# Optimization experiments

Hardware: AMD Instinct MI355X
Metric: run time of the kernel (lower is better)

Reference implementation:

```python
import jax, jax.numpy as jnp
import numpy as np

N_WAY = 64

def setup_inputs() -> dict:
    key = jax.random.key(0)
    k1, k2, k3, k4 = jax.random.split(key, 4)
    S, Q, F, D = 1024, 16384, 2048, 512
    xs = jax.random.normal(k1, (S, F), dtype=jnp.float32)
    ys = jax.random.randint(k2, (S,), 0, N_WAY, dtype=jnp.int64)
    xq = jax.random.normal(k3, (Q, F), dtype=jnp.float32)
    W = jax.random.normal(k4, (F, D), dtype=jnp.float32) * 0.02
    b = jnp.zeros((D,), dtype=jnp.float32)
    return {"xs": xs, "ys": ys, "xq": xq, "W": W, "b": b}

def reference(xs, ys, xq, W, b):
    # encoder: linear projection [*, F] -> [*, D]
    z_s = xs @ W + b            # [S, D]
    z_q = xq @ W + b            # [Q, D]
    # class prototypes: segment mean over support embeddings -> [N_way, D]
    counts = jax.ops.segment_sum(jnp.ones_like(ys, dtype=z_s.dtype), ys, num_segments=N_WAY)
    proto = jax.ops.segment_sum(z_s, ys, num_segments=N_WAY) / jnp.clip(counts, 1.0)[:, None]
    # pairwise squared euclidean distance (expand + pow + sum), [Q, N_way]
    diff = z_q[:, None, :] - proto[None, :, :]   # [Q, N_way, D]
    dists = jnp.sum(diff * diff, axis=-1)
    return -dists
```

## Files before the change

kernel.cpp:

```cpp
#include <hip/hip_runtime.h>


typedef __attribute__((ext_vector_type(8))) short short8;
typedef __attribute__((ext_vector_type(4))) float floatx4;

#define S_ROWS 1024
#define F_DIM  2048
#define D_DIM  512
#define NWAY   64
#define Q_ROWS 16384

static __device__ __forceinline__ unsigned short f2bf(float f) {
  unsigned int u = __float_as_uint(f);
  u += 0x7FFF + ((u >> 16) & 1);
  return (unsigned short)(u >> 16);
}
static __device__ __forceinline__ float bf2f(unsigned short s) {
  return __uint_as_float(((unsigned int)s) << 16);
}
static __device__ __forceinline__ unsigned int pack_bf2(float x, float y) {
  unsigned int ux = __float_as_uint(x) + 0x8000u;
  unsigned int uy = __float_as_uint(y) + 0x8000u;
  return __builtin_amdgcn_perm(uy, ux, 0x07060302u);
}
static __device__ __forceinline__ void load_lds16(const unsigned short* g, unsigned short* l) {
  __builtin_amdgcn_global_load_lds((const __attribute__((address_space(1))) unsigned int*)g,
                                   (__attribute__((address_space(3))) unsigned int*)l,
                                   16, 0, 0);
}

__global__ __launch_bounds__(256) void k_prep(const float* __restrict__ W,
                                              unsigned short* __restrict__ Wt,
                                              const int* __restrict__ ys,
                                              int* __restrict__ order,
                                              int* __restrict__ starts,
                                              float* __restrict__ counts) {
  __shared__ unsigned short t[64][65];
  __shared__ int cnt[NWAY];
  __shared__ int st[NWAY + 1];
  __shared__ int wp[NWAY];
  int bx = blockIdx.x;
  int tid = threadIdx.x;
  if (bx < 256) {
    int f0 = (bx >> 3) << 6;
    int d0 = (bx & 7) << 6;
    for (int j = 0; j < 16; j++) {
      int lin = j * 256 + tid;
      int fl = lin >> 6, dl = lin & 63;
      t[fl][dl] = f2bf(W[(size_t)(f0 + fl) * D_DIM + d0 + dl]);
    }
    __syncthreads();
    for (int j = 0; j < 16; j++) {
      int lin = j * 256 + tid;
      int dl = lin >> 6, fl = lin & 63;
      Wt[(size_t)(d0 + dl) * F_DIM + f0 + fl] = t[fl][dl];
    }
  } else {
    if (tid < NWAY) cnt[tid] = 0;
    __syncthreads();
    for (int j = tid; j < S_ROWS; j += 256) atomicAdd(&cnt[ys[j]], 1);
    __syncthreads();
    if (tid == 0) {
      int a = 0;
      for (int c = 0; c < NWAY; c++) { st[c] = a; wp[c] = a; a += cnt[c]; }
      st[NWAY] = a;
    }
    __syncthreads();
    for (int j = tid; j < S_ROWS; j += 256) {
      int c = ys[j];
      int p = atomicAdd(&wp[c], 1);
      order[p] = j;
    }
    if (tid < NWAY) counts[tid] = (float)cnt[tid];
    if (tid < NWAY + 1) starts[tid] = st[tid];
  }
}

__global__ __launch_bounds__(256) void k1_csum(const float* __restrict__ xs,
                                               const int* __restrict__ order,
                                               const int* __restrict__ starts,
                                               float* __restrict__ csum) {
  __shared__ int lord[S_ROWS];
  int c = blockIdx.x >> 1;
  int tid = threadIdx.x;
  int s = starts[c], e = starts[c + 1];
  int len = e - s;
  for (int j = tid; j < len; j += 256) lord[j] = order[s + j];
  __syncthreads();
  int f0 = (blockIdx.x & 1) * 1024 + tid * 4;
  float4 a = {0.f, 0.f, 0.f, 0.f};
  for (int i = 0; i < len; i++) {
    float4 v = *(const float4*)&xs[(size_t)lord[i] * F_DIM + f0];
    a.x += v.x; a.y += v.y; a.z += v.z; a.w += v.w;
  }
  *(float4*)&csum[(size_t)c * F_DIM + f0] = a;
}

__global__ __launch_bounds__(256) void k2p(const float* __restrict__ W,
                                           const float* __restrict__ csum,
                                           float* __restrict__ proto_part) {
  __shared__ __align__(16) float csl[64 * 65];
  __shared__ __align__(16) float wch[64 * 64];
  int bx = blockIdx.x;
  int fg = bx >> 3, dc = bx & 7;
  int d0 = dc * 64;
  int tid = threadIdx.x;
  int c = tid >> 2, dq = (tid & 3) * 16;
  floatx4 a0 = {0.f,0.f,0.f,0.f}, a1 = a0, a2 = a0, a3 = a0;
  for (int fsub = 0; fsub < 4; fsub++) {
    int f0 = (fg * 4 + fsub) * 64;
    __syncthreads();
    for (int idx = tid; idx < 4096; idx += 256) {
      int r = idx >> 6, q = idx & 63;
      csl[r * 65 + q] = csum[(size_t)r * F_DIM + f0 + q];
      wch[idx] = W[(size_t)(f0 + r) * D_DIM + d0 + q];
    }
    __syncthreads();
#pragma unroll 4
    for (int f = 0; f < 64; f++) {
      float s = csl[c * 65 + f];
      const floatx4* wr = (const floatx4*)&wch[f * 64 + dq];
      floatx4 w0 = wr[0], w1 = wr[1], w2 = wr[2], w3 = wr[3];
      a0 += s * w0; a1 += s * w1; a2 += s * w2; a3 += s * w3;
    }
  }
  float* dst = &proto_part[((size_t)fg * NWAY + c) * D_DIM + d0 + dq];
  *(floatx4*)&dst[0]  = a0;
  *(floatx4*)&dst[4]  = a1;
  *(floatx4*)&dst[8]  = a2;
  *(floatx4*)&dst[12] = a3;
}

__global__ __launch_bounds__(256) void k_pfin(const float* __restrict__ proto_part,
                                              const float* __restrict__ b,
                                              const float* __restrict__ counts,
                                              unsigned short* __restrict__ proto_bf,
                                              float* __restrict__ pnorm) {
  __shared__ float red[256];
  int n = blockIdx.x, tid = threadIdx.x;
  float cntv = counts[n];
  float inv = 1.f / fmaxf(cntv, 1.f);
  float part = 0.f;
#pragma unroll
  for (int h = 0; h < 2; h++) {
    int d = h * 256 + tid;
    float raw = 0.f;
#pragma unroll
    for (int p = 0; p < 8; p++)
      raw += proto_part[((size_t)p * NWAY + n) * D_DIM + d];
    float pv = (raw + cntv * b[d]) * inv;
    unsigned short hh = f2bf(pv);
    proto_bf[(size_t)n * D_DIM + d] = hh;
    float q = bf2f(hh);
    part += q * q;
  }
  red[tid] = part;
  __syncthreads();
  for (int s = 128; s > 0; s >>= 1) {
    if (tid < s) red[tid] += red[tid + s];
    __syncthreads();
  }
  if (tid == 0) pnorm[n] = red[0];
}

__global__ __launch_bounds__(256) void k3_gemm(const float* __restrict__ xq,
                                               const unsigned short* __restrict__ Wt,
                                               const float* __restrict__ b,
                                               unsigned short* __restrict__ zbuf) {
  __shared__ __align__(16) unsigned short lA[128 * 64];
  __shared__ __align__(16) unsigned short lB[128 * 64];
  int tid = threadIdx.x;
  int bx = blockIdx.x;
  int xcd = bx & 7;
  int wg = xcd * 64 + (bx >> 3);
  int mt = wg >> 2;
  int n0 = (wg & 3) * 128;

  int wave = tid >> 6, lane = tid & 63;
  int wr = wave >> 1, wc = wave & 1;
  int lrow = lane & 15, lquad = lane >> 4;

  const float* Ab = xq + (size_t)mt * 128 * F_DIM;

  floatx4 acc[4][4];
#pragma unroll
  for (int i = 0; i < 4; i++)
#pragma unroll
    for (int j = 0; j < 4; j++) acc[i][j] = (floatx4){0.f, 0.f, 0.f, 0.f};

  int sr = tid >> 3, skq = tid & 7;
  const float* ag = Ab + (size_t)sr * F_DIM + skq * 8;
  const unsigned short* bg = Wt + (size_t)(n0 + sr) * F_DIM + skq * 8;

  for (int k0 = 0; k0 < F_DIM; k0 += 64) {
#pragma unroll
    for (int i = 0; i < 4; i++)
      load_lds16(bg + (size_t)i * 32 * F_DIM + k0, &lB[(i * 256 + wave * 64) * 8]);
#pragma unroll
    for (int p = 0; p < 4; p++) {
      const float* gp = ag + (size_t)p * 32 * F_DIM + k0;
      float4 v0 = *(const float4*)gp;
      float4 v1 = *(const float4*)(gp + 4);
      uint4 w;
      w.x = pack_bf2(v0.x, v0.y); w.y = pack_bf2(v0.z, v0.w);
      w.z = pack_bf2(v1.x, v1.y); w.w = pack_bf2(v1.z, v1.w);
      *(uint4*)&lA[(p * 256 + tid) * 8] = w;
    }
    __syncthreads();
#pragma unroll
    for (int s = 0; s < 2; s++) {
      short8 af[4], bfr[4];
#pragma unroll
      for (int i = 0; i < 4; i++)
        af[i] = *(const short8*)&lA[(wr * 64 + i * 16 + lrow) * 64 + s * 32 + lquad * 8];
#pragma unroll
      for (int j = 0; j < 4; j++)
        bfr[j] = *(const short8*)&lB[(wc * 64 + j * 16 + lrow) * 64 + s * 32 + lquad * 8];
#pragma unroll
      for (int i = 0; i < 4; i++)
#pragma unroll
        for (int j = 0; j < 4; j++)
          acc[i][j] = __builtin_amdgcn_mfma_f32_16x16x32_bf16(af[i], bfr[j], acc[i][j], 0, 0, 0);
    }
    __syncthreads();
  }

  size_t zr0 = (size_t)mt * 128;
#pragma unroll
  for (int j = 0; j < 4; j++) {
    int col = n0 + wc * 64 + j * 16 + lrow;
    float bb = b[col];
#pragma unroll
    for (int i = 0; i < 4; i++) {
#pragma unroll
      for (int r = 0; r < 4; r++) {
        int row = wr * 64 + i * 16 + lquad * 4 + r;
        zbuf[(zr0 + row) * D_DIM + col] = f2bf(acc[i][j][r] + bb);
      }
    }
  }
}

__global__ __launch_bounds__(256) void k5_dist(const unsigned short* __restrict__ zbuf,
                                               const unsigned short* __restrict__ proto_bf,
                                               const float* __restrict__ pnorm,
                                               float* __restrict__ out) {
  __shared__ float S[64 * 65];
  __shared__ float qn_l[64];
  __shared__ float pn_l[64];
  int tid = threadIdx.x;
  int q0 = blockIdx.x * 64;
  int wave = tid >> 6, lane = tid & 63;
  int lrow = lane & 15, lquad = lane >> 4;

  for (int i = tid; i < 64 * 65; i += 256) S[i] = 0.f;
  if (tid < 64) { qn_l[tid] = 0.f; pn_l[tid] = pnorm[tid]; }
  __syncthreads();

  floatx4 acc[4][4];
#pragma unroll
  for (int i = 0; i < 4; i++)
#pragma unroll
    for (int j = 0; j < 4; j++) acc[i][j] = (floatx4){0.f, 0.f, 0.f, 0.f};
  float qsq[4] = {0.f, 0.f, 0.f, 0.f};

  int kbase = wave * 128;
#pragma unroll
  for (int kk = 0; kk < 4; kk++) {
    int k0 = kbase + kk * 32;
    short8 af[4], bfr[4];
#pragma unroll
    for (int i = 0; i < 4; i++)
      af[i] = *(const short8*)&zbuf[(size_t)(q0 + i * 16 + lrow) * D_DIM + k0 + lquad * 8];
#pragma unroll
    for (int j = 0; j < 4; j++)
      bfr[j] = *(const short8*)&proto_bf[(size_t)(j * 16 + lrow) * D_DIM + k0 + lquad * 8];
#pragma unroll
    for (int i = 0; i < 4; i++) {
#pragma unroll
      for (int h = 0; h < 8; h++) {
        float v = bf2f((unsigned short)af[i][h]);
        qsq[i] += v * v;
      }
#pragma unroll
      for (int j = 0; j < 4; j++)
        acc[i][j] = __builtin_amdgcn_mfma_f32_16x16x32_bf16(af[i], bfr[j], acc[i][j], 0, 0, 0);
    }
  }

#pragma unroll
  for (int i = 0; i < 4; i++) {
    float s = qsq[i];
    s += __shfl_xor(s, 16);
    s += __shfl_xor(s, 32);
    if (lquad == 0) atomicAdd(&qn_l[i * 16 + lrow], s);
  }
#pragma unroll
  for (int i = 0; i < 4; i++)
#pragma unroll
    for (int j = 0; j < 4; j++)
#pragma unroll
      for (int r = 0; r < 4; r++)
        atomicAdd(&S[(i * 16 + lquad * 4 + r) * 65 + j * 16 + lrow], acc[i][j][r]);
  __syncthreads();

  int row = tid >> 2, c0 = (tid & 3) * 16;
  float qv = qn_l[row];
#pragma unroll
  for (int u = 0; u < 4; u++) {
    float4 o;
    int cb = c0 + u * 4;
    o.x = 2.f * S[row * 65 + cb + 0] - qv - pn_l[cb + 0];
    o.y = 2.f * S[row * 65 + cb + 1] - qv - pn_l[cb + 1];
    o.z = 2.f * S[row * 65 + cb + 2] - qv - pn_l[cb + 2];
    o.w = 2.f * S[row * 65 + cb + 3] - qv - pn_l[cb + 3];
    *(float4*)&out[(size_t)(q0 + row) * NWAY + cb] = o;
  }
}

extern "C" void kernel_launch(void* const* d_in, const int* in_sizes, int n_in,
                              void* d_out, int out_size, void* d_ws, size_t ws_size,
                              hipStream_t stream) {
  const float* xs = (const float*)d_in[0];
  const int* ys = (const int*)d_in[1];
  const float* xq = (const float*)d_in[2];
  const float* W = (const float*)d_in[3];
  const float* b = (const float*)d_in[4];
  float* out = (float*)d_out;
  char* ws = (char*)d_ws;

  size_t off = 0;
  auto take = [&](size_t bytes) -> char* {
    char* r = ws + off;
    off += (bytes + 255) & ~(size_t)255;
    return r;
  };
  unsigned short* Wt = (unsigned short*)take((size_t)D_DIM * F_DIM * 2);
  float* csum = (float*)take((size_t)NWAY * F_DIM * 4);
  float* proto_part = (float*)take((size_t)8 * NWAY * D_DIM * 4);
  unsigned short* proto_bf = (unsigned short*)take((size_t)NWAY * D_DIM * 2);
  float* counts = (float*)take(NWAY * 4);
  float* pnorm = (float*)take(NWAY * 4);
  int* order = (int*)take(S_ROWS * 4);
  int* starts = (int*)take((NWAY + 1) * 4);
  unsigned short* zbuf = (unsigned short*)take((size_t)Q_ROWS * D_DIM * 2);

  if (off > ws_size) return;

  k_prep<<<257, 256, 0, stream>>>(W, Wt, ys, order, starts, counts);
  k1_csum<<<128, 256, 0, stream>>>(xs, order, starts, csum);
  k2p<<<64, 256, 0, stream>>>(W, csum, proto_part);
  k_pfin<<<NWAY, 256, 0, stream>>>(proto_part, b, counts, proto_bf, pnorm);
  k3_gemm<<<512, 256, 0, stream>>>(xq, Wt, b, zbuf);
  k5_dist<<<256, 256, 0, stream>>>(zbuf, proto_bf, pnorm, out);
}
```

Before: 299.7 us.

## Fuse all stages into one persistent kernel with grid barriers and fused distance

Six launches become a single persistent kernel of 512 blocks that separates the prototype-building stages with a software grid barrier built on atomics. The distance computation is fused into the GEMM epilogue: each block stages its bf16 z tile in LDS, computes partial query norms and partial dot products against its 128-column slice of the prototypes, and adds the result into the zeroed output with atomicAdd. The intermediate z buffer and its global round trip go away, along with the launch gaps. In exchange the code relies on all 512 blocks being co-resident for the spin barrier, and does four float atomics per output element.

```diff
diff --git a/kernel.cpp b/kernel.cpp
--- a/kernel.cpp
+++ b/kernel.cpp
@@ -9,6 +9,8 @@
 #define D_DIM  512
 #define NWAY   64
 #define Q_ROWS 16384
+#define NBLK   512
+#define ZS_LD  136
 
 static __device__ __forceinline__ unsigned short f2bf(float f) {
   unsigned int u = __float_as_uint(f);
@@ -29,19 +31,45 @@
                                    16, 0, 0);
 }
 
-__global__ __launch_bounds__(256) void k_prep(const float* __restrict__ W,
-                                              unsigned short* __restrict__ Wt,
-                                              const int* __restrict__ ys,
-                                              int* __restrict__ order,
-                                              int* __restrict__ starts,
-                                              float* __restrict__ counts) {
-  __shared__ unsigned short t[64][65];
-  __shared__ int cnt[NWAY];
-  __shared__ int st[NWAY + 1];
-  __shared__ int wp[NWAY];
+static __device__ __forceinline__ void grid_sync(int* bcnt, int* bgen) {
+  __syncthreads();
+  if (threadIdx.x == 0) {
+    __threadfence();
+    int g = atomicAdd(bgen, 0);
+    if (atomicAdd(bcnt, 1) == NBLK - 1) {
+      atomicExch(bcnt, 0);
+      __threadfence();
+      atomicAdd(bgen, 1);
+    } else {
+      while (atomicAdd(bgen, 0) == g) __builtin_amdgcn_s_sleep(8);
+    }
+    __threadfence();
+  }
+  __syncthreads();
+}
+
+__global__ __launch_bounds__(256, 2) void mega(
+    const float* __restrict__ xs, const int* __restrict__ ys,
+    const float* __restrict__ xq, const float* __restrict__ W,
+    const float* __restrict__ b, float* __restrict__ out,
+    unsigned short* __restrict__ Wt, float* __restrict__ csum,
+    float* __restrict__ proto_part, unsigned short* __restrict__ proto_bf,
+    float* __restrict__ pnorm_part, int* __restrict__ order,
+    int* __restrict__ starts, int* __restrict__ bar) {
+  __shared__ __align__(16) char smem[35584];
   int bx = blockIdx.x;
   int tid = threadIdx.x;
+  int* bcnt = bar;
+  int* bgen = bar + 1;
+
+  {
+    float4 zz = {0.f, 0.f, 0.f, 0.f};
+    float* dst = out + (size_t)bx * 2048 + tid * 8;
+    *(float4*)dst = zz;
+    *(float4*)(dst + 4) = zz;
+  }
   if (bx < 256) {
+    unsigned short(*t)[65] = (unsigned short(*)[65])smem;
     int f0 = (bx >> 3) << 6;
     int d0 = (bx & 7) << 6;
     for (int j = 0; j < 16; j++) {
@@ -55,7 +83,10 @@
       int dl = lin >> 6, fl = lin & 63;
       Wt[(size_t)(d0 + dl) * F_DIM + f0 + fl] = t[fl][dl];
     }
-  } else {
+  } else if (bx == 256) {
+    int* cnt = (int*)smem;
+    int* st = (int*)(smem + 256);
+    int* wp = (int*)(smem + 520);
     if (tid < NWAY) cnt[tid] = 0;
     __syncthreads();
     for (int j = tid; j < S_ROWS; j += 256) atomicAdd(&cnt[ys[j]], 1);
@@ -71,250 +102,220 @@
       int p = atomicAdd(&wp[c], 1);
       order[p] = j;
     }
-    if (tid < NWAY) counts[tid] = (float)cnt[tid];
     if (tid < NWAY + 1) starts[tid] = st[tid];
   }
-}
-
-__global__ __launch_bounds__(256) void k1_csum(const float* __restrict__ xs,
-                                               const int* __restrict__ order,
-                                               const int* __restrict__ starts,
-                                               float* __restrict__ csum) {
-  __shared__ int lord[S_ROWS];
-  int c = blockIdx.x >> 1;
-  int tid = threadIdx.x;
-  int s = starts[c], e = starts[c + 1];
-  int len = e - s;
-  for (int j = tid; j < len; j += 256) lord[j] = order[s + j];
-  __syncthreads();
-  int f0 = (blockIdx.x & 1) * 1024 + tid * 4;
-  float4 a = {0.f, 0.f, 0.f, 0.f};
-  for (int i = 0; i < len; i++) {
-    float4 v = *(const float4*)&xs[(size_t)lord[i] * F_DIM + f0];
-    a.x += v.x; a.y += v.y; a.z += v.z; a.w += v.w;
-  }
-  *(float4*)&csum[(size_t)c * F_DIM + f0] = a;
-}
-
-__global__ __launch_bounds__(256) void k2p(const float* __restrict__ W,
-                                           const float* __restrict__ csum,
-                                           float* __restrict__ proto_part) {
-  __shared__ __align__(16) float csl[64 * 65];
-  __shared__ __align__(16) float wch[64 * 64];
-  int bx = blockIdx.x;
-  int fg = bx >> 3, dc = bx & 7;
-  int d0 = dc * 64;
-  int tid = threadIdx.x;
-  int c = tid >> 2, dq = (tid & 3) * 16;
-  floatx4 a0 = {0.f,0.f,0.f,0.f}, a1 = a0, a2 = a0, a3 = a0;
-  for (int fsub = 0; fsub < 4; fsub++) {
-    int f0 = (fg * 4 + fsub) * 64;
-    __syncthreads();
-    for (int idx = tid; idx < 4096; idx += 256) {
-      int r = idx >> 6, q = idx & 63;
-      csl[r * 65 + q] = csum[(size_t)r * F_DIM + f0 + q];
-      wch[idx] = W[(size_t)(f0 + r) * D_DIM + d0 + q];
-    }
-    __syncthreads();
+  grid_sync(bcnt, bgen);
+
+  if (bx < 128) {
+    int* lord = (int*)smem;
+    int c = bx >> 1;
+    int s = starts[c], e = starts[c + 1];
+    int len = e - s;
+    for (int j = tid; j < len; j += 256) lord[j] = order[s + j];
+    __syncthreads();
+    int f0 = (bx & 1) * 1024 + tid * 4;
+    float4 a = {0.f, 0.f, 0.f, 0.f};
+    for (int i = 0; i < len; i++) {
+      float4 v = *(const float4*)&xs[(size_t)lord[i] * F_DIM + f0];
+      a.x += v.x; a.y += v.y; a.z += v.z; a.w += v.w;
+    }
+    *(float4*)&csum[(size_t)c * F_DIM + f0] = a;
+  }
+  grid_sync(bcnt, bgen);
+
+  if (bx < 64) {
+    float* csl = (float*)smem;
+    float* wch = (float*)(smem + 16640);
+    int fg = bx >> 3, dc = bx & 7;
+    int d0 = dc * 64;
+    int c = tid >> 2, dq = (tid & 3) * 16;
+    floatx4 a0 = {0.f, 0.f, 0.f, 0.f}, a1 = a0, a2 = a0, a3 = a0;
+    for (int fsub = 0; fsub < 4; fsub++) {
+      int f0 = (fg * 4 + fsub) * 64;
+      __syncthreads();
+      for (int idx = tid; idx < 4096; idx += 256) {
+        int r = idx >> 6, q = idx & 63;
+        csl[r * 65 + q] = csum[(size_t)r * F_DIM + f0 + q];
+        wch[idx] = W[(size_t)(f0 + r) * D_DIM + d0 + q];
+      }
+      __syncthreads();
 #pragma unroll 4
-    for (int f = 0; f < 64; f++) {
-      float s = csl[c * 65 + f];
-      const floatx4* wr = (const floatx4*)&wch[f * 64 + dq];
-      floatx4 w0 = wr[0], w1 = wr[1], w2 = wr[2], w3 = wr[3];
-      a0 += s * w0; a1 += s * w1; a2 += s * w2; a3 += s * w3;
-    }
-  }
-  float* dst = &proto_part[((size_t)fg * NWAY + c) * D_DIM + d0 + dq];
-  *(floatx4*)&dst[0]  = a0;
-  *(floatx4*)&dst[4]  = a1;
-  *(floatx4*)&dst[8]  = a2;
-  *(floatx4*)&dst[12] = a3;
-}
-
-__global__ __launch_bounds__(256) void k_pfin(const float* __restrict__ proto_part,
-                                              const float* __restrict__ b,
-                                              const float* __restrict__ counts,
-                                              unsigned short* __restrict__ proto_bf,
-                                              float* __restrict__ pnorm) {
-  __shared__ float red[256];
-  int n = blockIdx.x, tid = threadIdx.x;
-  float cntv = counts[n];
-  float inv = 1.f / fmaxf(cntv, 1.f);
-  float part = 0.f;
-#pragma unroll
-  for (int h = 0; h < 2; h++) {
-    int d = h * 256 + tid;
-    float raw = 0.f;
-#pragma unroll
-    for (int p = 0; p < 8; p++)
-      raw += proto_part[((size_t)p * NWAY + n) * D_DIM + d];
-    float pv = (raw + cntv * b[d]) * inv;
-    unsigned short hh = f2bf(pv);
-    proto_bf[(size_t)n * D_DIM + d] = hh;
-    float q = bf2f(hh);
-    part += q * q;
-  }
-  red[tid] = part;
-  __syncthreads();
-  for (int s = 128; s > 0; s >>= 1) {
-    if (tid < s) red[tid] += red[tid + s];
-    __syncthreads();
-  }
-  if (tid == 0) pnorm[n] = red[0];
-}
-
-__global__ __launch_bounds__(256) void k3_gemm(const float* __restrict__ xq,
-                                               const unsigned short* __restrict__ Wt,
-                                               const float* __restrict__ b,
-                                               unsigned short* __restrict__ zbuf) {
-  __shared__ __align__(16) unsigned short lA[128 * 64];
-  __shared__ __align__(16) unsigned short lB[128 * 64];
-  int tid = threadIdx.x;
-  int bx = blockIdx.x;
-  int xcd = bx & 7;
-  int wg = xcd * 64 + (bx >> 3);
-  int mt = wg >> 2;
-  int n0 = (wg & 3) * 128;
-
-  int wave = tid >> 6, lane = tid & 63;
-  int wr = wave >> 1, wc = wave & 1;
-  int lrow = lane & 15, lquad = lane >> 4;
-
-  const float* Ab = xq + (size_t)mt * 128 * F_DIM;
-
-  floatx4 acc[4][4];
-#pragma unroll
-  for (int i = 0; i < 4; i++)
-#pragma unroll
-    for (int j = 0; j < 4; j++) acc[i][j] = (floatx4){0.f, 0.f, 0.f, 0.f};
-
-  int sr = tid >> 3, skq = tid & 7;
-  const float* ag = Ab + (size_t)sr * F_DIM + skq * 8;
-  const unsigned short* bg = Wt + (size_t)(n0 + sr) * F_DIM + skq * 8;
-
-  for (int k0 = 0; k0 < F_DIM; k0 += 64) {
+      for (int f = 0; f < 64; f++) {
+        float sv = csl[c * 65 + f];
+        const floatx4* wr = (const floatx4*)&wch[f * 64 + dq];
+        floatx4 w0 = wr[0], w1 = wr[1], w2 = wr[2], w3 = wr[3];
+        a0 += sv * w0; a1 += sv * w1; a2 += sv * w2; a3 += sv * w3;
+      }
+    }
+    float* dst = &proto_part[((size_t)fg * NWAY + c) * D_DIM + d0 + dq];
+    *(floatx4*)&dst[0] = a0;
+    *(floatx4*)&dst[4] = a1;
+    *(floatx4*)&dst[8] = a2;
+    *(floatx4*)&dst[12] = a3;
+  }
+  grid_sync(bcnt, bgen);
+
+  if (bx < 64) {
+    float* red = (float*)smem;
+    int n = bx;
+    float cntv = (float)(starts[n + 1] - starts[n]);
+    float inv = 1.f / fmaxf(cntv, 1.f);
+#pragma unroll
+    for (int h = 0; h < 2; h++) {
+      int d = h * 256 + tid;
+      float raw = 0.f;
+#pragma unroll
+      for (int p = 0; p < 8; p++)
+        raw += proto_part[((size_t)p * NWAY + n) * D_DIM + d];
+      float pv = (raw + cntv * b[d]) * inv;
+      unsigned short hh = f2bf(pv);
+      proto_bf[(size_t)n * D_DIM + d] = hh;
+      float q = bf2f(hh);
+      __syncthreads();
+      red[tid] = q * q;
+      __syncthreads();
+      for (int s = 64; s > 0; s >>= 1) {
+        if ((tid & 127) < s) red[tid] += red[tid + s];
+        __syncthreads();
+      }
+      if (tid == 0) pnorm_part[(h * 2 + 0) * 64 + n] = red[0];
+      if (tid == 128) pnorm_part[(h * 2 + 1) * 64 + n] = red[128];
+    }
+  }
+  grid_sync(bcnt, bgen);
+
+  {
+    unsigned short* lA = (unsigned short*)smem;
+    unsigned short* lB = (unsigned short*)(smem + 16384);
+    unsigned short* zs = (unsigned short*)smem;
+    float* qnf = (float*)(smem + 34816);
+    float* pnl = (float*)(smem + 35328);
+
+    int xcd = bx & 7;
+    int wg = xcd * 64 + (bx >> 3);
+    int mt = wg >> 2;
+    int slice = wg & 3;
+    int n0 = slice * 128;
+
+    int wave = tid >> 6, lane = tid & 63;
+    int wr = wave >> 1, wc = wave & 1;
+    int lrow = lane & 15, lquad = lane >> 4;
+
+    const float* Ab = xq + (size_t)mt * 128 * F_DIM;
+
+    floatx4 acc[4][4];
 #pragma unroll
     for (int i = 0; i < 4; i++)
-      load_lds16(bg + (size_t)i * 32 * F_DIM + k0, &lB[(i * 256 + wave * 64) * 8]);
-#pragma unroll
-    for (int p = 0; p < 4; p++) {
-      const float* gp = ag + (size_t)p * 32 * F_DIM + k0;
-      float4 v0 = *(const float4*)gp;
-      float4 v1 = *(const float4*)(gp + 4);
-      uint4 w;
-      w.x = pack_bf2(v0.x, v0.y); w.y = pack_bf2(v0.z, v0.w);
-      w.z = pack_bf2(v1.x, v1.y); w.w = pack_bf2(v1.z, v1.w);
-      *(uint4*)&lA[(p * 256 + tid) * 8] = w;
-    }
-    __syncthreads();
-#pragma unroll
-    for (int s = 0; s < 2; s++) {
-      short8 af[4], bfr[4];
+#pragma unroll
+      for (int j = 0; j < 4; j++) acc[i][j] = (floatx4){0.f, 0.f, 0.f, 0.f};
+
+    int sr = tid >> 3, skq = tid & 7;
+    const float* ag = Ab + (size_t)sr * F_DIM + skq * 8;
+    const unsigned short* bg = Wt + (size_t)(n0 + sr) * F_DIM + skq * 8;
+
+    for (int k0 = 0; k0 < F_DIM; k0 += 64) {
 #pragma unroll
       for (int i = 0; i < 4; i++)
-        af[i] = *(const short8*)&lA[(wr * 64 + i * 16 + lrow) * 64 + s * 32 + lquad * 8];
+        load_lds16(bg + (size_t)i * 32 * F_DIM + k0, &lB[(i * 256 + wave * 64) * 8]);
+#pragma unroll
+      for (int p = 0; p < 4; p++) {
+        const float* gp = ag + (size_t)p * 32 * F_DIM + k0;
+        float4 v0 = *(const float4*)gp;
+        float4 v1 = *(const float4*)(gp + 4);
+        uint4 w;
+        w.x = pack_bf2(v0.x, v0.y); w.y = pack_bf2(v0.z, v0.w);
+        w.z = pack_bf2(v1.x, v1.y); w.w = pack_bf2(v1.z, v1.w);
+        *(uint4*)&lA[(p * 256 + tid) * 8] = w;
+      }
+      __syncthreads();
+#pragma unroll
+      for (int s = 0; s < 2; s++) {
+        short8 af[4], bfr[4];
+#pragma unroll
+        for (int i = 0; i < 4; i++)
+          af[i] = *(const short8*)&lA[(wr * 64 + i * 16 + lrow) * 64 + s * 32 + lquad * 8];
+#pragma unroll
+        for (int j = 0; j < 4; j++)
+          bfr[j] = *(const short8*)&lB[(wc * 64 + j * 16 + lrow) * 64 + s * 32 + lquad * 8];
+#pragma unroll
+        for (int i = 0; i < 4; i++)
+#pragma unroll
+          for (int j = 0; j < 4; j++)
+            acc[i][j] = __builtin_amdgcn_mfma_f32_16x16x32_bf16(af[i], bfr[j], acc[i][j], 0, 0, 0);
+      }
+      __syncthreads();
+    }
+
+    if (tid < 128) qnf[tid] = 0.f;
+    if (tid < 64) pnl[tid] = pnorm_part[slice * 64 + tid];
+    __syncthreads();
+
+#pragma unroll
+    for (int i = 0; i < 4; i++) {
+      float rn[4] = {0.f, 0.f, 0.f, 0.f};
+#pragma unroll
+      for (int j = 0; j < 4; j++) {
+        int col = wc * 64 + j * 16 + lrow;
+        float bb = b[n0 + col];
+#pragma unroll
+        for (int r = 0; r < 4; r++) {
+          int row = wr * 64 + i * 16 + lquad * 4 + r;
+          float v = acc[i][j][r] + bb;
+          unsigned short h = f2bf(v);
+          zs[row * ZS_LD + col] = h;
+          float vq = bf2f(h);
+          rn[r] += vq * vq;
+        }
+      }
+#pragma unroll
+      for (int r = 0; r < 4; r++) {
+        float s2 = rn[r];
+        s2 += __shfl_xor(s2, 1, 16);
+        s2 += __shfl_xor(s2, 2, 16);
+        s2 += __shfl_xor(s2, 4, 16);
+        s2 += __shfl_xor(s2, 8, 16);
+        if (lrow == 0) atomicAdd(&qnf[wr * 64 + i * 16 + lquad * 4 + r], s2);
+      }
+    }
+    __syncthreads();
+
+    floatx4 acc2[2][4];
+#pragma unroll
+    for (int i = 0; i < 2; i++)
+#pragma unroll
+      for (int j = 0; j < 4; j++) acc2[i][j] = (floatx4){0.f, 0.f, 0.f, 0.f};
+
+#pragma unroll
+    for (int ks = 0; ks < 4; ks++) {
+      short8 af2[2], bp[4];
+#pragma unroll
+      for (int i = 0; i < 2; i++)
+        af2[i] = *(const short8*)&zs[(wave * 32 + i * 16 + lrow) * ZS_LD + ks * 32 + lquad * 8];
 #pragma unroll
       for (int j = 0; j < 4; j++)
-        bfr[j] = *(const short8*)&lB[(wc * 64 + j * 16 + lrow) * 64 + s * 32 + lquad * 8];
-#pragma unroll
-      for (int i = 0; i < 4; i++)
+        bp[j] = *(const short8*)&proto_bf[(size_t)(j * 16 + lrow) * D_DIM + n0 + ks * 32 + lquad * 8];
+#pragma unroll
+      for (int i = 0; i < 2; i++)
 #pragma unroll
         for (int j = 0; j < 4; j++)
-          acc[i][j] = __builtin_amdgcn_mfma_f32_16x16x32_bf16(af[i], bfr[j], acc[i][j], 0, 0, 0);
-    }
-    __syncthreads();
-  }
-
-  size_t zr0 = (size_t)mt * 128;
-#pragma unroll
-  for (int j = 0; j < 4; j++) {
-    int col = n0 + wc * 64 + j * 16 + lrow;
-    float bb = b[col];
-#pragma unroll
-    for (int i = 0; i < 4; i++) {
-#pragma unroll
-      for (int r = 0; r < 4; r++) {
-        int row = wr * 64 + i * 16 + lquad * 4 + r;
-        zbuf[(zr0 + row) * D_DIM + col] = f2bf(acc[i][j][r] + bb);
-      }
-    }
-  }
-}
-
-__global__ __launch_bounds__(256) void k5_dist(const unsigned short* __restrict__ zbuf,
-                                               const unsigned short* __restrict__ proto_bf,
-                                               const float* __restrict__ pnorm,
-                                               float* __restrict__ out) {
-  __shared__ float S[64 * 65];
-  __shared__ float qn_l[64];
-  __shared__ float pn_l[64];
-  int tid = threadIdx.x;
-  int q0 = blockIdx.x * 64;
-  int wave = tid >> 6, lane = tid & 63;
-  int lrow = lane & 15, lquad = lane >> 4;
-
-  for (int i = tid; i < 64 * 65; i += 256) S[i] = 0.f;
-  if (tid < 64) { qn_l[tid] = 0.f; pn_l[tid] = pnorm[tid]; }
-  __syncthreads();
-
-  floatx4 acc[4][4];
-#pragma unroll
-  for (int i = 0; i < 4; i++)
-#pragma unroll
-    for (int j = 0; j < 4; j++) acc[i][j] = (floatx4){0.f, 0.f, 0.f, 0.f};
-  float qsq[4] = {0.f, 0.f, 0.f, 0.f};
-
-  int kbase = wave * 128;
-#pragma unroll
-  for (int kk = 0; kk < 4; kk++) {
-    int k0 = kbase + kk * 32;
-    short8 af[4], bfr[4];
-#pragma unroll
-    for (int i = 0; i < 4; i++)
-      af[i] = *(const short8*)&zbuf[(size_t)(q0 + i * 16 + lrow) * D_DIM + k0 + lquad * 8];
-#pragma unroll
-    for (int j = 0; j < 4; j++)
-      bfr[j] = *(const short8*)&proto_bf[(size_t)(j * 16 + lrow) * D_DIM + k0 + lquad * 8];
-#pragma unroll
-    for (int i = 0; i < 4; i++) {
-#pragma unroll
-      for (int h = 0; h < 8; h++) {
-        float v = bf2f((unsigned short)af[i][h]);
-        qsq[i] += v * v;
-      }
-#pragma unroll
-      for (int j = 0; j < 4; j++)
-        acc[i][j] = __builtin_amdgcn_mfma_f32_16x16x32_bf16(af[i], bfr[j], acc[i][j], 0, 0, 0);
-    }
-  }
-
-#pragma unroll
-  for (int i = 0; i < 4; i++) {
-    float s = qsq[i];
-    s += __shfl_xor(s, 16);
-    s += __shfl_xor(s, 32);
-    if (lquad == 0) atomicAdd(&qn_l[i * 16 + lrow], s);
-  }
-#pragma unroll
-  for (int i = 0; i < 4; i++)
-#pragma unroll
-    for (int j = 0; j < 4; j++)
-#pragma unroll
-      for (int r = 0; r < 4; r++)
-        atomicAdd(&S[(i * 16 + lquad * 4 + r) * 65 + j * 16 + lrow], acc[i][j][r]);
-  __syncthreads();
-
-  int row = tid >> 2, c0 = (tid & 3) * 16;
-  float qv = qn_l[row];
-#pragma unroll
-  for (int u = 0; u < 4; u++) {
-    float4 o;
-    int cb = c0 + u * 4;
-    o.x = 2.f * S[row * 65 + cb + 0] - qv - pn_l[cb + 0];
-    o.y = 2.f * S[row * 65 + cb + 1] - qv - pn_l[cb + 1];
-    o.z = 2.f * S[row * 65 + cb + 2] - qv - pn_l[cb + 2];
-    o.w = 2.f * S[row * 65 + cb + 3] - qv - pn_l[cb + 3];
-    *(float4*)&out[(size_t)(q0 + row) * NWAY + cb] = o;
+          acc2[i][j] = __builtin_amdgcn_mfma_f32_16x16x32_bf16(af2[i], bp[j], acc2[i][j], 0, 0, 0);
+    }
+
+    size_t qbase = (size_t)mt * 128;
+#pragma unroll
+    for (int i = 0; i < 2; i++) {
+#pragma unroll
+      for (int j = 0; j < 4; j++) {
+        int c = j * 16 + lrow;
+        float pn = pnl[c];
+#pragma unroll
+        for (int r = 0; r < 4; r++) {
+          int ql = wave * 32 + i * 16 + lquad * 4 + r;
+          float val = 2.f * acc2[i][j][r] - qnf[ql] - pn;
+          atomicAdd(&out[(qbase + ql) * NWAY + c], val);
+        }
+      }
+    }
   }
 }
 
@@ -339,18 +340,14 @@
   float* csum = (float*)take((size_t)NWAY * F_DIM * 4);
   float* proto_part = (float*)take((size_t)8 * NWAY * D_DIM * 4);
   unsigned short* proto_bf = (unsigned short*)take((size_t)NWAY * D_DIM * 2);
-  float* counts = (float*)take(NWAY * 4);
-  float* pnorm = (float*)take(NWAY * 4);
+  float* pnorm_part = (float*)take(4 * NWAY * 4);
   int* order = (int*)take(S_ROWS * 4);
   int* starts = (int*)take((NWAY + 1) * 4);
-  unsigned short* zbuf = (unsigned short*)take((size_t)Q_ROWS * D_DIM * 2);
+  int* bar = (int*)take(256);
 
   if (off > ws_size) return;
 
-  k_prep<<<257, 256, 0, stream>>>(W, Wt, ys, order, starts, counts);
-  k1_csum<<<128, 256, 0, stream>>>(xs, order, starts, csum);
-  k2p<<<64, 256, 0, stream>>>(W, csum, proto_part);
-  k_pfin<<<NWAY, 256, 0, stream>>>(proto_part, b, counts, proto_bf, pnorm);
-  k3_gemm<<<512, 256, 0, stream>>>(xq, Wt, b, zbuf);
-  k5_dist<<<256, 256, 0, stream>>>(zbuf, proto_bf, pnorm, out);
-}
+  hipMemsetAsync(bar, 0, 8, stream);
+  mega<<<NBLK, 256, 0, stream>>>(xs, ys, xq, W, b, out, Wt, csum, proto_part,
+                                 proto_bf, pnorm_part, order, starts, bar);
+}
```

After: 498.5 us. +66.4%, slower.
